# Optimization experiments

Hardware: AMD Instinct MI355X
Metric: run time of the kernel (lower is better)

Reference implementation:

```python
import jax, jax.numpy as jnp
import numpy as np

NUM_STREAMS = 4
DIM = 256
SINKHORN_ITERS = 10
SINKHORN_TAU = 0.05


def sinkhorn_log(logits, num_iters=SINKHORN_ITERS, tau=SINKHORN_TAU):
    n = logits.shape[-1]
    z = logits / tau
    log_marginal = -jnp.log(jnp.asarray(float(n), dtype=logits.dtype))

    def body(carry, _):
        u, v = carry
        u = log_marginal - jax.scipy.special.logsumexp(z + v[None, :], axis=1)
        v = log_marginal - jax.scipy.special.logsumexp(z + u[:, None], axis=0)
        return (u, v), None

    u0 = jnp.zeros((n,), dtype=z.dtype)
    v0 = jnp.zeros((n,), dtype=z.dtype)
    (u, v), _ = jax.lax.scan(body, (u0, v0), None, length=num_iters)
    return jnp.exp(z + u[:, None] + v[None, :]) * n


def setup_inputs() -> dict:
    key = jax.random.key(0)
    k_res, k_w = jax.random.split(key)
    B = 65536
    residuals = jax.random.normal(k_res, (B, NUM_STREAMS, DIM), dtype=jnp.float32)
    # h_res_logits: -8 everywhere, 0 on diagonal (as in __init__)
    h_res_logits = jnp.full((NUM_STREAMS, NUM_STREAMS), -8.0, dtype=jnp.float32)
    h_res_logits = h_res_logits.at[jnp.arange(NUM_STREAMS), jnp.arange(NUM_STREAMS)].set(0.0)
    # h_pre_logits: -8 everywhere, 0 at init_residual_index=0
    h_pre_logits = jnp.full((NUM_STREAMS,), -8.0, dtype=jnp.float32).at[0].set(0.0)
    h_post_logits = jnp.zeros((NUM_STREAMS,), dtype=jnp.float32)
    # branch Linear(dim, dim, bias=False): weight (out, in), y = x @ W.T
    bound = 1.0 / np.sqrt(DIM)
    W_branch = jax.random.uniform(k_w, (DIM, DIM), dtype=jnp.float32, minval=-bound, maxval=bound)
    return {
        "residuals": residuals,
        "h_res_logits": h_res_logits,
        "h_pre_logits": h_pre_logits,
        "h_post_logits": h_post_logits,
        "W_branch": W_branch,
    }


def reference(residuals, h_res_logits, h_pre_logits, h_post_logits, W_branch):
    # residuals: (B, S, D)
    h_res = sinkhorn_log(h_res_logits)                     # (S, S) doubly-stochastic * n
    h_pre = jax.nn.softmax(h_pre_logits)                   # (S,)
    h_post = jax.nn.softmax(h_post_logits)                 # (S,)
    residuals_mixed = jnp.einsum('st,bsd->btd', h_res, residuals)
    branch_input = jnp.einsum('s,bsd->bd', h_pre, residuals)
    branch_output = branch_input @ W_branch.T              # (B, D)
    depth_out = jnp.einsum('bd,s->bsd', branch_output, h_post)
    return residuals_mixed + depth_out
```

## Files before the change

### kernel.cpp

```cpp
#include <hip/hip_runtime.h>

#define NSTREAMS 4
#define DIM 256
#define BM 16
#define NTHREADS 1024
#define TILES 16

typedef __attribute__((ext_vector_type(8))) short short8;
typedef __attribute__((ext_vector_type(4))) float f32x4;

static __device__ __forceinline__ short f2bf(float x) {
    union { float f; unsigned int u; } c; c.f = x;
    unsigned int u = c.u;
    unsigned int lsb = (u >> 16) & 1u;
    u += 0x7fffu + lsb;
    return (short)(u >> 16);
}
static __device__ __forceinline__ int2 f2bf4(float4 v) {
    unsigned int lo, hi;
    asm("v_cvt_pk_bf16_f32 %0, %1, %2" : "=v"(lo) : "v"(v.x), "v"(v.y));
    asm("v_cvt_pk_bf16_f32 %0, %1, %2" : "=v"(hi) : "v"(v.z), "v"(v.w));
    int2 r; r.x = (int)lo; r.y = (int)hi;
    return r;
}

static __device__ __forceinline__ float rfl(float x) {
    int i = __builtin_amdgcn_readfirstlane(__builtin_bit_cast(int, x));
    return __builtin_bit_cast(float, i);
}

static __device__ __forceinline__ void barrier_lgkm() {
    asm volatile("s_waitcnt lgkmcnt(0)\n\ts_barrier" ::: "memory");
}

static __device__ void compute_h(const float* __restrict__ hres_l,
                                 const float* __restrict__ hpre_l,
                                 const float* __restrict__ hpost_l,
                                 float* h_out) {
    const float inv_tau = 1.0f / 0.05f;
    float z[4][4];
    for (int i = 0; i < 4; ++i)
        for (int j = 0; j < 4; ++j)
            z[i][j] = hres_l[i * 4 + j] * inv_tau;
    float u[4] = {0.f, 0.f, 0.f, 0.f};
    float v[4] = {0.f, 0.f, 0.f, 0.f};
    const float logm = -logf(4.0f);
    for (int it = 0; it < 10; ++it) {
        for (int i = 0; i < 4; ++i) {
            float m = -1e30f;
            for (int j = 0; j < 4; ++j) m = fmaxf(m, z[i][j] + v[j]);
            float ss = 0.f;
            for (int j = 0; j < 4; ++j) ss += expf(z[i][j] + v[j] - m);
            u[i] = logm - (m + logf(ss));
        }
        for (int j = 0; j < 4; ++j) {
            float m = -1e30f;
            for (int i = 0; i < 4; ++i) m = fmaxf(m, z[i][j] + u[i]);
            float ss = 0.f;
            for (int i = 0; i < 4; ++i) ss += expf(z[i][j] + u[i] - m);
            v[j] = logm - (m + logf(ss));
        }
    }
    for (int i = 0; i < 4; ++i)
        for (int j = 0; j < 4; ++j)
            h_out[i * 4 + j] = expf(z[i][j] + u[i] + v[j]) * 4.0f;
    {
        float m = fmaxf(fmaxf(hpre_l[0], hpre_l[1]), fmaxf(hpre_l[2], hpre_l[3]));
        float e0 = expf(hpre_l[0] - m), e1 = expf(hpre_l[1] - m);
        float e2 = expf(hpre_l[2] - m), e3 = expf(hpre_l[3] - m);
        float ss = e0 + e1 + e2 + e3;
        h_out[16] = e0 / ss; h_out[17] = e1 / ss; h_out[18] = e2 / ss; h_out[19] = e3 / ss;
    }
    {
        float m = fmaxf(fmaxf(hpost_l[0], hpost_l[1]), fmaxf(hpost_l[2], hpost_l[3]));
        float e0 = expf(hpost_l[0] - m), e1 = expf(hpost_l[1] - m);
        float e2 = expf(hpost_l[2] - m), e3 = expf(hpost_l[3] - m);
        float ss = e0 + e1 + e2 + e3;
        h_out[20] = e0 / ss; h_out[21] = e1 / ss; h_out[22] = e2 / ss; h_out[23] = e3 / ss;
    }
}

__global__ void prep_h_kernel(const float* __restrict__ hres_l,
                              const float* __restrict__ hpre_l,
                              const float* __restrict__ hpost_l,
                              float* __restrict__ ws) {
    if (threadIdx.x == 0) compute_h(hres_l, hpre_l, hpost_l, ws);
}

__global__ __launch_bounds__(256) void prep_wh_kernel(const float* __restrict__ Wb,
                                                      short* __restrict__ wbf,
                                                      const float* __restrict__ hres_l,
                                                      const float* __restrict__ hpre_l,
                                                      const float* __restrict__ hpost_l,
                                                      float* __restrict__ ws_h) {
    int idx = blockIdx.x * 256 + threadIdx.x;
    float4 v = reinterpret_cast<const float4*>(Wb)[idx];
    reinterpret_cast<int2*>(wbf)[idx] = f2bf4(v);
    if (blockIdx.x == 0 && threadIdx.x == 0)
        compute_h(hres_l, hpre_l, hpost_l, ws_h);
}

template <bool USE_WSW>
__global__ __launch_bounds__(NTHREADS, 1) void fused_kernel(
    const float* __restrict__ res,
    const float* __restrict__ Wb,
    const short* __restrict__ wbf,
    const float* __restrict__ hptr,
    const float* __restrict__ hres_l,
    const float* __restrict__ hpre_l,
    const float* __restrict__ hpost_l,
    float* __restrict__ out)
{
    __shared__ __align__(16) short W_lds[DIM * DIM];
    __shared__ __align__(16) short bi_lds[BM][DIM + 8];
    __shared__ __align__(16) float bo_lds[BM][DIM + 4];
    __shared__ float h_sh[24];

    const int t  = threadIdx.x;
    const int d4 = t & 63;
    const int r0 = t >> 6;
    const int w  = t >> 6;
    const int l  = t & 63;
    const int lr = l & 15;
    const int lk = l >> 4;

    const long tile0 = (long)blockIdx.x * TILES;
    const long rowbase = (tile0 * BM + r0) * (NSTREAMS * DIM);

    float4 A0, A1, A2, A3;
    {
        const float4* p = reinterpret_cast<const float4*>(res + rowbase) + d4;
        A0 = p[0]; A1 = p[64]; A2 = p[128]; A3 = p[192];
    }

    #pragma unroll
    for (int i = 0; i < 8; ++i) {
        int c = t * 8 + i;
        int row = c >> 5;
        int koff = (c & 31) * 16;
        int dst = (row << 9) | (koff ^ ((row & 7) << 4));
        int4 wv;
        if (USE_WSW) {
            wv = reinterpret_cast<const int4*>(wbf)[c];
        } else {
            const float4* wp = reinterpret_cast<const float4*>(Wb) + c * 2;
            float4 wa = wp[0], wb2 = wp[1];
            int2 loq = f2bf4(wa), hiq = f2bf4(wb2);
            wv.x = loq.x; wv.y = loq.y; wv.z = hiq.x; wv.w = hiq.y;
        }
        *reinterpret_cast<int4*>(reinterpret_cast<char*>(W_lds) + dst) = wv;
    }

    if (hptr) {
        if (t < 24) h_sh[t] = hptr[t];
    } else if (t == 0) {
        compute_h(hres_l, hpre_l, hpost_l, h_sh);
    }
    barrier_lgkm();

    const float hp0 = rfl(h_sh[16]), hp1 = rfl(h_sh[17]);
    const float hp2 = rfl(h_sh[18]), hp3 = rfl(h_sh[19]);
    float hres[4][4];
    #pragma unroll
    for (int s = 0; s < 4; ++s)
        #pragma unroll
        for (int tt = 0; tt < 4; ++tt)
            hres[s][tt] = rfl(h_sh[s * 4 + tt]);
    float hq[4] = {rfl(h_sh[20]), rfl(h_sh[21]), rfl(h_sh[22]), rfl(h_sh[23])};

    float4 B0, B1, B2, B3;
    {
        const float4* p = reinterpret_cast<const float4*>(
            res + rowbase + 1 * BM * (NSTREAMS * DIM)) + d4;
        B0 = p[0]; B1 = p[64]; B2 = p[128]; B3 = p[192];
    }

    float4 opart[4];
    {
        float4 bi;
        bi.x = hp0 * A0.x + hp1 * A1.x + hp2 * A2.x + hp3 * A3.x;
        bi.y = hp0 * A0.y + hp1 * A1.y + hp2 * A2.y + hp3 * A3.y;
        bi.z = hp0 * A0.z + hp1 * A1.z + hp2 * A2.z + hp3 * A3.z;
        bi.w = hp0 * A0.w + hp1 * A1.w + hp2 * A2.w + hp3 * A3.w;
        *reinterpret_cast<int2*>(&bi_lds[r0][d4 * 4]) = f2bf4(bi);
        #pragma unroll
        for (int tt = 0; tt < 4; ++tt) {
            opart[tt].x = hres[0][tt] * A0.x + hres[1][tt] * A1.x + hres[2][tt] * A2.x + hres[3][tt] * A3.x;
            opart[tt].y = hres[0][tt] * A0.y + hres[1][tt] * A1.y + hres[2][tt] * A2.y + hres[3][tt] * A3.y;
            opart[tt].z = hres[0][tt] * A0.z + hres[1][tt] * A1.z + hres[2][tt] * A2.z + hres[3][tt] * A3.z;
            opart[tt].w = hres[0][tt] * A0.w + hres[1][tt] * A1.w + hres[2][tt] * A2.w + hres[3][tt] * A3.w;
        }
    }
    barrier_lgkm();

    const int dcol = w * 16 + lr;
    const char* wbase = reinterpret_cast<const char*>(W_lds) + (dcol << 9);
    const int dswz = (dcol & 7) << 4;
    const long tstride = (long)BM * (NSTREAMS * DIM);

    for (int ti = 0; ti < TILES; ti += 2) {
        {
            if (ti + 2 < TILES) {
                const float4* p = reinterpret_cast<const float4*>(
                    res + rowbase + (ti + 2) * tstride) + d4;
                A0 = p[0]; A1 = p[64]; A2 = p[128]; A3 = p[192];
            }
            __builtin_amdgcn_sched_barrier(0);
            f32x4 acc = {0.f, 0.f, 0.f, 0.f};
            #pragma unroll
            for (int k0 = 0; k0 < DIM; k0 += 32) {
                short8 a = *reinterpret_cast<const short8*>(&bi_lds[lr][k0 + lk * 8]);
                short8 b = *reinterpret_cast<const short8*>(
                    wbase + ((k0 * 2 + lk * 16) ^ dswz));
                acc = __builtin_amdgcn_mfma_f32_16x16x32_bf16(a, b, acc, 0, 0, 0);
            }
            #pragma unroll
            for (int j = 0; j < 4; ++j)
                bo_lds[lk * 4 + j][dcol] = acc[j];
            barrier_lgkm();
            {
                float4 bo = *reinterpret_cast<const float4*>(&bo_lds[r0][d4 * 4]);
                float* obase = out + (((tile0 + ti) * BM + r0) * 4) * DIM + d4 * 4;
                #pragma unroll
                for (int tt = 0; tt < 4; ++tt) {
                    float4 o;
                    o.x = opart[tt].x + hq[tt] * bo.x;
                    o.y = opart[tt].y + hq[tt] * bo.y;
                    o.z = opart[tt].z + hq[tt] * bo.z;
                    o.w = opart[tt].w + hq[tt] * bo.w;
                    *reinterpret_cast<float4*>(obase + tt * DIM) = o;
                }
            }
            {
                float4 bi;
                bi.x = hp0 * B0.x + hp1 * B1.x + hp2 * B2.x + hp3 * B3.x;
                bi.y = hp0 * B0.y + hp1 * B1.y + hp2 * B2.y + hp3 * B3.y;
                bi.z = hp0 * B0.z + hp1 * B1.z + hp2 * B2.z + hp3 * B3.z;
                bi.w = hp0 * B0.w + hp1 * B1.w + hp2 * B2.w + hp3 * B3.w;
                *reinterpret_cast<int2*>(&bi_lds[r0][d4 * 4]) = f2bf4(bi);
                #pragma unroll
                for (int tt = 0; tt < 4; ++tt) {
                    opart[tt].x = hres[0][tt] * B0.x + hres[1][tt] * B1.x + hres[2][tt] * B2.x + hres[3][tt] * B3.x;
                    opart[tt].y = hres[0][tt] * B0.y + hres[1][tt] * B1.y + hres[2][tt] * B2.y + hres[3][tt] * B3.y;
                    opart[tt].z = hres[0][tt] * B0.z + hres[1][tt] * B1.z + hres[2][tt] * B2.z + hres[3][tt] * B3.z;
                    opart[tt].w = hres[0][tt] * B0.w + hres[1][tt] * B1.w + hres[2][tt] * B2.w + hres[3][tt] * B3.w;
                }
            }
            barrier_lgkm();
        }
        {
            if (ti + 3 < TILES) {
                const float4* p = reinterpret_cast<const float4*>(
                    res + rowbase + (ti + 3) * tstride) + d4;
                B0 = p[0]; B1 = p[64]; B2 = p[128]; B3 = p[192];
            }
            __builtin_amdgcn_sched_barrier(0);
            f32x4 acc = {0.f, 0.f, 0.f, 0.f};
            #pragma unroll
            for (int k0 = 0; k0 < DIM; k0 += 32) {
                short8 a = *reinterpret_cast<const short8*>(&bi_lds[lr][k0 + lk * 8]);
                short8 b = *reinterpret_cast<const short8*>(
                    wbase + ((k0 * 2 + lk * 16) ^ dswz));
                acc = __builtin_amdgcn_mfma_f32_16x16x32_bf16(a, b, acc, 0, 0, 0);
            }
            #pragma unroll
            for (int j = 0; j < 4; ++j)
                bo_lds[lk * 4 + j][dcol] = acc[j];
            barrier_lgkm();
            {
                float4 bo = *reinterpret_cast<const float4*>(&bo_lds[r0][d4 * 4]);
                float* obase = out + (((tile0 + ti + 1) * BM + r0) * 4) * DIM + d4 * 4;
                #pragma unroll
                for (int tt = 0; tt < 4; ++tt) {
                    float4 o;
                    o.x = opart[tt].x + hq[tt] * bo.x;
                    o.y = opart[tt].y + hq[tt] * bo.y;
                    o.z = opart[tt].z + hq[tt] * bo.z;
                    o.w = opart[tt].w + hq[tt] * bo.w;
                    *reinterpret_cast<float4*>(obase + tt * DIM) = o;
                }
            }
            if (ti + 2 < TILES) {
                float4 bi;
                bi.x = hp0 * A0.x + hp1 * A1.x + hp2 * A2.x + hp3 * A3.x;
                bi.y = hp0 * A0.y + hp1 * A1.y + hp2 * A2.y + hp3 * A3.y;
                bi.z = hp0 * A0.z + hp1 * A1.z + hp2 * A2.z + hp3 * A3.z;
                bi.w = hp0 * A0.w + hp1 * A1.w + hp2 * A2.w + hp3 * A3.w;
                *reinterpret_cast<int2*>(&bi_lds[r0][d4 * 4]) = f2bf4(bi);
                #pragma unroll
                for (int tt = 0; tt < 4; ++tt) {
                    opart[tt].x = hres[0][tt] * A0.x + hres[1][tt] * A1.x + hres[2][tt] * A2.x + hres[3][tt] * A3.x;
                    opart[tt].y = hres[0][tt] * A0.y + hres[1][tt] * A1.y + hres[2][tt] * A2.y + hres[3][tt] * A3.y;
                    opart[tt].z = hres[0][tt] * A0.z + hres[1][tt] * A1.z + hres[2][tt] * A2.z + hres[3][tt] * A3.z;
                    opart[tt].w = hres[0][tt] * A0.w + hres[1][tt] * A1.w + hres[2][tt] * A2.w + hres[3][tt] * A3.w;
                }
            }
            barrier_lgkm();
        }
    }
}

extern "C" void kernel_launch(void* const* d_in, const int* in_sizes, int n_in,
                              void* d_out, int out_size, void* d_ws, size_t ws_size,
                              hipStream_t stream) {
    const float* res     = (const float*)d_in[0];
    const float* hres_l  = (const float*)d_in[1];
    const float* hpre_l  = (const float*)d_in[2];
    const float* hpost_l = (const float*)d_in[3];
    const float* Wb      = (const float*)d_in[4];
    float* out = (float*)d_out;

    const int Btot = in_sizes[0] / (NSTREAMS * DIM);
    const int grid = Btot / (BM * TILES);

    const size_t W_OFF = 256;
    const size_t need_h = 24 * sizeof(float);
    const size_t need_w = W_OFF + (size_t)DIM * DIM * sizeof(short);
    const bool has_h = ws_size >= need_h;
    const bool has_w = ws_size >= need_w;

    float* ws_h = (float*)d_ws;
    short* ws_w = (short*)((char*)d_ws + W_OFF);

    if (has_w) {
        prep_wh_kernel<<<(DIM * DIM / 4) / 256, 256, 0, stream>>>(
            Wb, ws_w, hres_l, hpre_l, hpost_l, ws_h);
        fused_kernel<true><<<grid, NTHREADS, 0, stream>>>(
            res, Wb, ws_w, ws_h, hres_l, hpre_l, hpost_l, out);
    } else if (has_h) {
        prep_h_kernel<<<1, 64, 0, stream>>>(hres_l, hpre_l, hpost_l, ws_h);
        fused_kernel<false><<<grid, NTHREADS, 0, stream>>>(
            res, Wb, nullptr, ws_h, hres_l, hpre_l, hpost_l, out);
    } else {
        fused_kernel<false><<<grid, NTHREADS, 0, stream>>>(
            res, Wb, nullptr, nullptr, hres_l, hpre_l, hpost_l, out);
    }
}
```

Baseline: 131.5 us.

## Swap MFMA operands so accumulators map to thread output layout, drop bo_lds

The GEMM operands are swapped so each lane's MFMA accumulator holds four consecutive output columns for one row. Thread-to-data mapping for loads and stores is changed to match, so the branch output is used straight from registers and the bo_lds staging round trip is removed. The bi buffer is double-buffered, which together with the lost staging step removes one barrier per tile. Global accesses become 16-byte segments per lane spread across rows instead of fully contiguous 1KB rows, which may reduce coalescing efficiency.

New measurement: 135.7 us. 1.03x slower.

```diff
diff --git a/kernel.cpp b/kernel.cpp
--- a/kernel.cpp
+++ b/kernel.cpp
@@ -112,26 +112,25 @@
     float* __restrict__ out)
 {
     __shared__ __align__(16) short W_lds[DIM * DIM];
-    __shared__ __align__(16) short bi_lds[BM][DIM + 8];
-    __shared__ __align__(16) float bo_lds[BM][DIM + 4];
+    __shared__ __align__(16) short bi_lds[2][BM][DIM + 8];
     __shared__ float h_sh[24];
 
     const int t  = threadIdx.x;
-    const int d4 = t & 63;
-    const int r0 = t >> 6;
     const int w  = t >> 6;
     const int l  = t & 63;
     const int lr = l & 15;
     const int lk = l >> 4;
 
     const long tile0 = (long)blockIdx.x * TILES;
-    const long rowbase = (tile0 * BM + r0) * (NSTREAMS * DIM);
+    const long tstride = (long)BM * (NSTREAMS * DIM);
+    const int d0 = w * 16 + lk * 4;
+    const float* rbase = res + (tile0 * BM + lr) * (NSTREAMS * DIM) + d0;
 
     float4 A0, A1, A2, A3;
-    {
-        const float4* p = reinterpret_cast<const float4*>(res + rowbase) + d4;
-        A0 = p[0]; A1 = p[64]; A2 = p[128]; A3 = p[192];
-    }
+    A0 = *reinterpret_cast<const float4*>(rbase + 0 * DIM);
+    A1 = *reinterpret_cast<const float4*>(rbase + 1 * DIM);
+    A2 = *reinterpret_cast<const float4*>(rbase + 2 * DIM);
+    A3 = *reinterpret_cast<const float4*>(rbase + 3 * DIM);
 
     #pragma unroll
     for (int i = 0; i < 8; ++i) {
@@ -170,9 +169,11 @@
 
     float4 B0, B1, B2, B3;
     {
-        const float4* p = reinterpret_cast<const float4*>(
-            res + rowbase + 1 * BM * (NSTREAMS * DIM)) + d4;
-        B0 = p[0]; B1 = p[64]; B2 = p[128]; B3 = p[192];
+        const float4* p0 = reinterpret_cast<const float4*>(rbase + tstride + 0 * DIM);
+        const float4* p1 = reinterpret_cast<const float4*>(rbase + tstride + 1 * DIM);
+        const float4* p2 = reinterpret_cast<const float4*>(rbase + tstride + 2 * DIM);
+        const float4* p3 = reinterpret_cast<const float4*>(rbase + tstride + 3 * DIM);
+        B0 = *p0; B1 = *p1; B2 = *p2; B3 = *p3;
     }
 
     float4 opart[4];
@@ -182,7 +183,7 @@
         bi.y = hp0 * A0.y + hp1 * A1.y + hp2 * A2.y + hp3 * A3.y;
         bi.z = hp0 * A0.z + hp1 * A1.z + hp2 * A2.z + hp3 * A3.z;
         bi.w = hp0 * A0.w + hp1 * A1.w + hp2 * A2.w + hp3 * A3.w;
-        *reinterpret_cast<int2*>(&bi_lds[r0][d4 * 4]) = f2bf4(bi);
+        *reinterpret_cast<int2*>(&bi_lds[0][lr][d0]) = f2bf4(bi);
         #pragma unroll
         for (int tt = 0; tt < 4; ++tt) {
             opart[tt].x = hres[0][tt] * A0.x + hres[1][tt] * A1.x + hres[2][tt] * A2.x + hres[3][tt] * A3.x;
@@ -196,38 +197,34 @@
     const int dcol = w * 16 + lr;
     const char* wbase = reinterpret_cast<const char*>(W_lds) + (dcol << 9);
     const int dswz = (dcol & 7) << 4;
-    const long tstride = (long)BM * (NSTREAMS * DIM);
 
     for (int ti = 0; ti < TILES; ti += 2) {
         {
             if (ti + 2 < TILES) {
-                const float4* p = reinterpret_cast<const float4*>(
-                    res + rowbase + (ti + 2) * tstride) + d4;
-                A0 = p[0]; A1 = p[64]; A2 = p[128]; A3 = p[192];
+                const float* rb = rbase + (ti + 2) * tstride;
+                A0 = *reinterpret_cast<const float4*>(rb + 0 * DIM);
+                A1 = *reinterpret_cast<const float4*>(rb + 1 * DIM);
+                A2 = *reinterpret_cast<const float4*>(rb + 2 * DIM);
+                A3 = *reinterpret_cast<const float4*>(rb + 3 * DIM);
             }
             __builtin_amdgcn_sched_barrier(0);
             f32x4 acc = {0.f, 0.f, 0.f, 0.f};
             #pragma unroll
             for (int k0 = 0; k0 < DIM; k0 += 32) {
-                short8 a = *reinterpret_cast<const short8*>(&bi_lds[lr][k0 + lk * 8]);
-                short8 b = *reinterpret_cast<const short8*>(
+                short8 bfrag = *reinterpret_cast<const short8*>(&bi_lds[0][lr][k0 + lk * 8]);
+                short8 afrag = *reinterpret_cast<const short8*>(
                     wbase + ((k0 * 2 + lk * 16) ^ dswz));
-                acc = __builtin_amdgcn_mfma_f32_16x16x32_bf16(a, b, acc, 0, 0, 0);
-            }
-            #pragma unroll
-            for (int j = 0; j < 4; ++j)
-                bo_lds[lk * 4 + j][dcol] = acc[j];
-            barrier_lgkm();
+                acc = __builtin_amdgcn_mfma_f32_16x16x32_bf16(afrag, bfrag, acc, 0, 0, 0);
+            }
             {
-                float4 bo = *reinterpret_cast<const float4*>(&bo_lds[r0][d4 * 4]);
-                float* obase = out + (((tile0 + ti) * BM + r0) * 4) * DIM + d4 * 4;
+                float* obase = out + (((tile0 + ti) * BM + lr) * 4) * DIM + d0;
                 #pragma unroll
                 for (int tt = 0; tt < 4; ++tt) {
                     float4 o;
-                    o.x = opart[tt].x + hq[tt] * bo.x;
-                    o.y = opart[tt].y + hq[tt] * bo.y;
-                    o.z = opart[tt].z + hq[tt] * bo.z;
-                    o.w = opart[tt].w + hq[tt] * bo.w;
+                    o.x = opart[tt].x + hq[tt] * acc[0];
+                    o.y = opart[tt].y + hq[tt] * acc[1];
+                    o.z = opart[tt].z + hq[tt] * acc[2];
+                    o.w = opart[tt].w + hq[tt] * acc[3];
                     *reinterpret_cast<float4*>(obase + tt * DIM) = o;
                 }
             }
@@ -237,7 +234,7 @@
                 bi.y = hp0 * B0.y + hp1 * B1.y + hp2 * B2.y + hp3 * B3.y;
                 bi.z = hp0 * B0.z + hp1 * B1.z + hp2 * B2.z + hp3 * B3.z;
                 bi.w = hp0 * B0.w + hp1 * B1.w + hp2 * B2.w + hp3 * B3.w;
-                *reinterpret_cast<int2*>(&bi_lds[r0][d4 * 4]) = f2bf4(bi);
+                *reinterpret_cast<int2*>(&bi_lds[1][lr][d0]) = f2bf4(bi);
                 #pragma unroll
                 for (int tt = 0; tt < 4; ++tt) {
                     opart[tt].x = hres[0][tt] * B0.x + hres[1][tt] * B1.x + hres[2][tt] * B2.x + hres[3][tt] * B3.x;
@@ -250,33 +247,30 @@
         }
         {
             if (ti + 3 < TILES) {
-                const float4* p = reinterpret_cast<const float4*>(
-                    res + rowbase + (ti + 3) * tstride) + d4;
-                B0 = p[0]; B1 = p[64]; B2 = p[128]; B3 = p[192];
+                const float* rb = rbase + (ti + 3) * tstride;
+                B0 = *reinterpret_cast<const float4*>(rb + 0 * DIM);
+                B1 = *reinterpret_cast<const float4*>(rb + 1 * DIM);
+                B2 = *reinterpret_cast<const float4*>(rb + 2 * DIM);
+                B3 = *reinterpret_cast<const float4*>(rb + 3 * DIM);
             }
             __builtin_amdgcn_sched_barrier(0);
             f32x4 acc = {0.f, 0.f, 0.f, 0.f};
             #pragma unroll
             for (int k0 = 0; k0 < DIM; k0 += 32) {
-                short8 a = *reinterpret_cast<const short8*>(&bi_lds[lr][k0 + lk * 8]);
-                short8 b = *reinterpret_cast<const short8*>(
+                short8 bfrag = *reinterpret_cast<const short8*>(&bi_lds[1][lr][k0 + lk * 8]);
+                short8 afrag = *reinterpret_cast<const short8*>(
                     wbase + ((k0 * 2 + lk * 16) ^ dswz));
-                acc = __builtin_amdgcn_mfma_f32_16x16x32_bf16(a, b, acc, 0, 0, 0);
-            }
-            #pragma unroll
-            for (int j = 0; j < 4; ++j)
-                bo_lds[lk * 4 + j][dcol] = acc[j];
-            barrier_lgkm();
+                acc = __builtin_amdgcn_mfma_f32_16x16x32_bf16(afrag, bfrag, acc, 0, 0, 0);
+            }
             {
-                float4 bo = *reinterpret_cast<const float4*>(&bo_lds[r0][d4 * 4]);
-                float* obase = out + (((tile0 + ti + 1) * BM + r0) * 4) * DIM + d4 * 4;
+                float* obase = out + (((tile0 + ti + 1) * BM + lr) * 4) * DIM + d0;
                 #pragma unroll
                 for (int tt = 0; tt < 4; ++tt) {
                     float4 o;
-                    o.x = opart[tt].x + hq[tt] * bo.x;
-                    o.y = opart[tt].y + hq[tt] * bo.y;
-                    o.z = opart[tt].z + hq[tt] * bo.z;
-                    o.w = opart[tt].w + hq[tt] * bo.w;
+                    o.x = opart[tt].x + hq[tt] * acc[0];
+                    o.y = opart[tt].y + hq[tt] * acc[1];
+                    o.z = opart[tt].z + hq[tt] * acc[2];
+                    o.w = opart[tt].w + hq[tt] * acc[3];
                     *reinterpret_cast<float4*>(obase + tt * DIM) = o;
                 }
             }
@@ -286,7 +280,7 @@
                 bi.y = hp0 * A0.y + hp1 * A1.y + hp2 * A2.y + hp3 * A3.y;
                 bi.z = hp0 * A0.z + hp1 * A1.z + hp2 * A2.z + hp3 * A3.z;
                 bi.w = hp0 * A0.w + hp1 * A1.w + hp2 * A2.w + hp3 * A3.w;
-                *reinterpret_cast<int2*>(&bi_lds[r0][d4 * 4]) = f2bf4(bi);
+                *reinterpret_cast<int2*>(&bi_lds[0][lr][d0]) = f2bf4(bi);
                 #pragma unroll
                 for (int tt = 0; tt < 4; ++tt) {
                     opart[tt].x = hres[0][tt] * A0.x + hres[1][tt] * A1.x + hres[2][tt] * A2.x + hres[3][tt] * A3.x;
```
